# Kernel tuning notes

Measured on AMD Instinct MI355X. Metric: run time of the kernel, lower is better.

Reference implementation:

```python
import jax, jax.numpy as jnp
import numpy as np
import math

B, S, D, H = 4, 1024, 1024, 16
DK = D // H
HID = 2 * D
EPS = 1e-5

def _lin(key, din, dout):
    kw, kb = jax.random.split(key)
    sc = 1.0 / math.sqrt(din)
    return (jax.random.uniform(kw, (din, dout), jnp.float32, -sc, sc),
            jax.random.uniform(kb, (dout,), jnp.float32, -sc, sc))

def setup_inputs() -> dict:
    key = jax.random.key(0)
    ks = jax.random.split(key, 10)
    x = jax.random.normal(ks[0], (B, S, D), jnp.float32)
    y = jax.random.normal(ks[1], (B, S, D), jnp.float32)
    # additive causal mask (zeros below/on diag, -1e9 above)
    mask = jnp.where(jnp.tril(jnp.ones((S, S), bool)), 0.0, -1e9).astype(jnp.float32)
    qkv_w, qkv_b = _lin(ks[2], D, 3 * D)
    ao_w, ao_b = _lin(ks[3], D, D)
    kv_w, kv_b = _lin(ks[4], D, 2 * D)
    q_w, q_b = _lin(ks[5], D, D)
    co_w, co_b = _lin(ks[6], D, D)
    fc1_w, fc1_b = _lin(ks[7], D, HID)
    fc2_w, fc2_b = _lin(ks[8], HID, D)
    g = jnp.ones((D,), jnp.float32)
    b = jnp.zeros((D,), jnp.float32)
    return dict(x=x, y=y, mask=mask,
                qkv_w=qkv_w, qkv_b=qkv_b, ao_w=ao_w, ao_b=ao_b,
                kv_w=kv_w, kv_b=kv_b, q_w=q_w, q_b=q_b, co_w=co_w, co_b=co_b,
                fc1_w=fc1_w, fc1_b=fc1_b, fc2_w=fc2_w, fc2_b=fc2_b,
                ln1_g=g, ln1_b=b, ln2_g=g, ln2_b=b, ln3_g=g, ln3_b=b)

def _heads(t):  # [B,S,D] -> [B,H,S,DK]
    return t.reshape(B, S, H, -1).transpose(0, 2, 1, 3)

def _merge(t):  # [B,H,S,DK] -> [B,S,D]
    return t.transpose(0, 2, 1, 3).reshape(B, S, D)

def _attn(q, k, v, mask):
    scores = jnp.einsum('bhqd,bhkd->bhqk', q, k) / math.sqrt(q.shape[-1])
    if mask is not None:
        scores = scores + mask
    p = jax.nn.softmax(scores, axis=-1)
    return jnp.einsum('bhqk,bhkd->bhqd', p, v)

def _ln(t, g, b):
    mu = jnp.mean(t, axis=-1, keepdims=True)
    var = jnp.mean(jnp.square(t - mu), axis=-1, keepdims=True)
    return (t - mu) / jnp.sqrt(var + EPS) * g + b

def reference(x, y, mask, qkv_w, qkv_b, ao_w, ao_b, kv_w, kv_b, q_w, q_b,
              co_w, co_b, fc1_w, fc1_b, fc2_w, fc2_b,
              ln1_g, ln1_b, ln2_g, ln2_b, ln3_g, ln3_b):
    # masked self-attention on y
    qkv = y @ qkv_w + qkv_b
    qh, kh, vh = jnp.split(_heads(qkv), 3, axis=-1)
    sa = _merge(_attn(qh, kh, vh, mask)) @ ao_w + ao_b
    y_att = _ln(sa + y, ln1_g, ln1_b)  # dropout is identity (eval)
    # cross-attention: kv from x, q from ORIGINAL y (as in source), no mask
    kv = _heads(x @ kv_w + kv_b)
    ck, cv = jnp.split(kv, 2, axis=-1)
    cq = _heads(y @ q_w + q_b)
    cross = _merge(_attn(cq, ck, cv, None)) @ co_w + co_b
    # quirk in source: LN applied BEFORE residual add here
    y_cross = _ln(cross, ln2_g, ln2_b) + y_att
    # feedforward (hidden = 2*d_model)
    ff = jax.nn.relu(y_cross @ fc1_w + fc1_b) @ fc2_w + fc2_b
    return _ln(ff + y_cross, ln3_g, ln3_b)
```

## Files before the change

### kernel.cpp

```cpp
#include <hip/hip_runtime.h>
#include <cstdint>
#include <cstddef>


#define DEV __device__ __forceinline__

typedef __bf16 bf16x8 __attribute__((ext_vector_type(8)));
typedef float f32x4 __attribute__((ext_vector_type(4)));

DEV float bf2f(uint16_t h) { return __builtin_bit_cast(float, (uint32_t)h << 16); }
DEV uint16_t f2bf(float f) {
  uint32_t u = __builtin_bit_cast(uint32_t, f);
  return (uint16_t)((u + 0x7fffu + ((u >> 16) & 1u)) >> 16);
}

DEV void gload16(const void* g, void* l) {
  __builtin_amdgcn_global_load_lds((const __attribute__((address_space(1))) void*)g,
                                   (__attribute__((address_space(3))) void*)l, 16, 0, 0);
}

__global__ __launch_bounds__(256) void cvt_f2b(const float* __restrict__ in,
                                               uint16_t* __restrict__ out, int n4) {
  const int i = blockIdx.x * 256 + threadIdx.x;
  if (i < n4) {
    const float4 v = ((const float4*)in)[i];
    const uint32_t w0 = (uint32_t)f2bf(v.x) | ((uint32_t)f2bf(v.y) << 16);
    const uint32_t w1 = (uint32_t)f2bf(v.z) | ((uint32_t)f2bf(v.w) << 16);
    ((uint2*)out)[i] = make_uint2(w0, w1);
  }
}

__global__ __launch_bounds__(256) void ktranspose(const float* __restrict__ W,
                                                  uint16_t* __restrict__ Wt,
                                                  int K, int N) {
  __shared__ float t[32][33];
  const int tx = threadIdx.x & 31, ty = threadIdx.x >> 5;
  const int n0 = blockIdx.x * 32, k0 = blockIdx.y * 32;
#pragma unroll
  for (int i = 0; i < 32; i += 8)
    t[ty + i][tx] = W[(size_t)(k0 + ty + i) * N + n0 + tx];
  __syncthreads();
#pragma unroll
  for (int i = 0; i < 32; i += 8)
    Wt[(size_t)(n0 + ty + i) * K + k0 + tx] = f2bf(t[tx][ty + i]);
}

enum { EP_QKV = 0, EP_RES_F32RES, EP_SCKV, EP_Q, EP_F32, EP_RELU, EP_RES_B16RES };

template <int EPI>
__global__ __launch_bounds__(256) void gemm_bt(const uint16_t* __restrict__ A,
                                               const uint16_t* __restrict__ Bt,
                                               const float* __restrict__ bias,
                                               void* __restrict__ out0,
                                               const void* __restrict__ res,
                                               int M, int N, int K) {
  __shared__ __align__(16) uint16_t As[128 * 32];
  __shared__ __align__(16) uint16_t Bs[128 * 32];
  const int tid = threadIdx.x;
  const int wid = tid >> 6, lane = tid & 63;
  const int g = lane >> 4, lr = lane & 15;
  const int wr = wid >> 1, wc = wid & 1;
  const int m0 = blockIdx.y * 128, n0 = blockIdx.x * 128;

  const char* Ab = (const char*)A;
  const char* Bb = (const char*)Bt;
  const size_t rs = (size_t)K * 2;

  const int rc = lane >> 2;
  const int scb = ((lane & 3) << 4) ^ ((rc & 3) << 4);

  int aoff[4], boff[4];
#pragma unroll
  for (int m = 0; m < 4; ++m) {
    const int row = wr * 64 + m * 16 + lr;
    aoff[m] = row * 64 + ((g * 16) ^ ((row & 3) << 4));
  }
#pragma unroll
  for (int n = 0; n < 4; ++n) {
    const int row = wc * 64 + n * 16 + lr;
    boff[n] = row * 64 + ((g * 16) ^ ((row & 3) << 4));
  }

  f32x4 acc[4][4] = {};
  const int nk = K >> 5;
  for (int kt = 0; kt < nk; ++kt) {
    __syncthreads();
#pragma unroll
    for (int i = 0; i < 2; ++i) {
      const int c = wid * 2 + i;
      gload16(Ab + (size_t)(m0 + c * 16 + rc) * rs + (size_t)kt * 64 + scb,
              (void*)((char*)As + c * 1024));
      gload16(Bb + (size_t)(n0 + c * 16 + rc) * rs + (size_t)kt * 64 + scb,
              (void*)((char*)Bs + c * 1024));
    }
    asm volatile("s_waitcnt vmcnt(0)" ::: "memory");
    __syncthreads();

    bf16x8 av[4], bv[4];
#pragma unroll
    for (int m = 0; m < 4; ++m) av[m] = *(const bf16x8*)((const char*)As + aoff[m]);
#pragma unroll
    for (int n = 0; n < 4; ++n) bv[n] = *(const bf16x8*)((const char*)Bs + boff[n]);
#pragma unroll
    for (int m = 0; m < 4; ++m)
#pragma unroll
      for (int n = 0; n < 4; ++n)
        acc[m][n] = __builtin_amdgcn_mfma_f32_16x16x32_bf16(av[m], bv[n], acc[m][n], 0, 0, 0);
  }

#pragma unroll
  for (int m = 0; m < 4; ++m) {
#pragma unroll
    for (int n = 0; n < 4; ++n) {
      const int gcol = n0 + wc * 64 + n * 16 + lr;
      const float bb = bias[gcol];
#pragma unroll
      for (int r = 0; r < 4; ++r) {
        const int grow = m0 + wr * 64 + m * 16 + g * 4 + r;
        float v = acc[m][n][r] + bb;
        if constexpr (EPI == EP_QKV) {
          const int b = grow >> 10, s = grow & 1023;
          const int h = gcol / 192;
          const int rr = gcol - h * 192;
          const int part = rr >> 6, d = rr & 63;
          const int bh = b * 16 + h;
          uint16_t* base = (uint16_t*)out0;
          if (part == 2)
            base[2u * 4194304u + ((size_t)bh * 64 + d) * 1024 + s] = f2bf(v);
          else
            base[(size_t)part * 4194304u + ((size_t)bh * 1024 + s) * 64 + d] = f2bf(v);
        } else if constexpr (EPI == EP_SCKV) {
          const int b = grow >> 10, s = grow & 1023;
          const int h = gcol >> 7, part = (gcol >> 6) & 1, d = gcol & 63;
          const int bh = b * 16 + h;
          uint16_t* base = (uint16_t*)out0;
          if (part == 0)
            base[((size_t)bh * 1024 + s) * 64 + d] = f2bf(v);
          else
            base[4194304u + ((size_t)bh * 64 + d) * 1024 + s] = f2bf(v);
        } else if constexpr (EPI == EP_Q) {
          const int b = grow >> 10, s = grow & 1023;
          const int h = gcol >> 6, d = gcol & 63;
          ((uint16_t*)out0)[((size_t)(b * 16 + h) * 1024 + s) * 64 + d] = f2bf(v);
        } else if constexpr (EPI == EP_RES_F32RES) {
          v += ((const float*)res)[(size_t)grow * N + gcol];
          ((float*)out0)[(size_t)grow * N + gcol] = v;
        } else if constexpr (EPI == EP_F32) {
          ((float*)out0)[(size_t)grow * N + gcol] = v;
        } else if constexpr (EPI == EP_RELU) {
          ((uint16_t*)out0)[(size_t)grow * N + gcol] = f2bf(v > 0.f ? v : 0.f);
        } else if constexpr (EPI == EP_RES_B16RES) {
          v += bf2f(((const uint16_t*)res)[(size_t)grow * N + gcol]);
          ((float*)out0)[(size_t)grow * N + gcol] = v;
        }
      }
    }
  }
}

template <bool CAUSAL>
__global__ __launch_bounds__(256) void attn_fused(const uint16_t* __restrict__ Qp,
                                                  const uint16_t* __restrict__ Kp,
                                                  const uint16_t* __restrict__ Vtp,
                                                  uint16_t* __restrict__ O) {
  __shared__ __align__(16) uint16_t Kl[64 * 64];
  __shared__ __align__(16) uint16_t Vl[64 * 64];
  __shared__ __align__(16) uint16_t Pl[4][16 * 64];
  const int tid = threadIdx.x, wid = tid >> 6, lane = tid & 63;
  const int g = lane >> 4, lr = lane & 15;
  const int qb = blockIdx.x, bh = blockIdx.y;
  const char* Qb = (const char*)(Qp + (size_t)bh * 65536);
  const char* Kb = (const char*)(Kp + (size_t)bh * 65536);
  const char* Vb = (const char*)(Vtp + (size_t)bh * 65536);
  const int q0 = qb * 64 + wid * 16;

  bf16x8 aq[2];
#pragma unroll
  for (int ks = 0; ks < 2; ++ks)
    aq[ks] = *(const bf16x8*)(Qb + ((size_t)(q0 + lr) * 64 + ks * 32 + g * 8) * 2);

  float m_run[4], l_run[4];
  f32x4 oacc[4] = {};
#pragma unroll
  for (int r = 0; r < 4; ++r) { m_run[r] = -1e30f; l_run[r] = 0.f; }

  const int rc = lane >> 3;
  const int scb = ((lane & 7) << 4) ^ (rc << 4);
  const int nkt = CAUSAL ? (qb + 1) : 16;

  for (int kt = 0; kt < nkt; ++kt) {
    __syncthreads();
#pragma unroll
    for (int i = 0; i < 2; ++i) {
      const int c = wid * 2 + i;
      gload16(Kb + (size_t)(kt * 64 + c * 8 + rc) * 128 + scb, (void*)((char*)Kl + c * 1024));
      gload16(Vb + (size_t)(c * 8 + rc) * 2048 + kt * 128 + scb, (void*)((char*)Vl + c * 1024));
    }
    asm volatile("s_waitcnt vmcnt(0)" ::: "memory");
    __syncthreads();

    f32x4 sc[4];
#pragma unroll
    for (int n = 0; n < 4; ++n) {
      f32x4 t = {};
#pragma unroll
      for (int ks = 0; ks < 2; ++ks) {
        const int row = n * 16 + lr;
        bf16x8 bk = *(const bf16x8*)((const char*)Kl + row * 128 +
                                     ((ks * 64 + g * 16) ^ ((row & 7) << 4)));
        t = __builtin_amdgcn_mfma_f32_16x16x32_bf16(aq[ks], bk, t, 0, 0, 0);
      }
      sc[n] = t;
    }
    float p[4][4];
#pragma unroll
    for (int n = 0; n < 4; ++n)
#pragma unroll
      for (int r = 0; r < 4; ++r) {
        float v = sc[n][r] * 0.125f;
        if (CAUSAL) {
          const int k_abs = kt * 64 + n * 16 + lr;
          const int q_abs = q0 + g * 4 + r;
          if (k_abs > q_abs) v = -1e9f;
        }
        p[n][r] = v;
      }
#pragma unroll
    for (int r = 0; r < 4; ++r) {
      float mx = fmaxf(fmaxf(p[0][r], p[1][r]), fmaxf(p[2][r], p[3][r]));
      mx = fmaxf(mx, __shfl_xor(mx, 1));
      mx = fmaxf(mx, __shfl_xor(mx, 2));
      mx = fmaxf(mx, __shfl_xor(mx, 4));
      mx = fmaxf(mx, __shfl_xor(mx, 8));
      const float mnew = fmaxf(m_run[r], mx);
      const float f = __expf(m_run[r] - mnew);
      m_run[r] = mnew;
      float ls = 0.f;
#pragma unroll
      for (int n = 0; n < 4; ++n) {
        const float e = __expf(p[n][r] - mnew);
        p[n][r] = e;
        ls += e;
      }
      ls += __shfl_xor(ls, 1);
      ls += __shfl_xor(ls, 2);
      ls += __shfl_xor(ls, 4);
      ls += __shfl_xor(ls, 8);
      l_run[r] = l_run[r] * f + ls;
#pragma unroll
      for (int n = 0; n < 4; ++n) oacc[n][r] *= f;
    }
    char* Pb = (char*)Pl[wid];
#pragma unroll
    for (int n = 0; n < 4; ++n)
#pragma unroll
      for (int r = 0; r < 4; ++r) {
        const int row = g * 4 + r;
        *(uint16_t*)(Pb + row * 128 + ((n * 32 + lr * 2) ^ ((row & 7) << 4))) = f2bf(p[n][r]);
      }
    asm volatile("s_waitcnt lgkmcnt(0)" ::: "memory");
#pragma unroll
    for (int ks = 0; ks < 2; ++ks) {
      bf16x8 pa = *(const bf16x8*)(Pb + lr * 128 + ((ks * 64 + g * 16) ^ ((lr & 7) << 4)));
#pragma unroll
      for (int n2 = 0; n2 < 4; ++n2) {
        const int row = n2 * 16 + lr;
        bf16x8 bv = *(const bf16x8*)((const char*)Vl + row * 128 +
                                     ((ks * 64 + g * 16) ^ ((row & 7) << 4)));
        oacc[n2] = __builtin_amdgcn_mfma_f32_16x16x32_bf16(pa, bv, oacc[n2], 0, 0, 0);
      }
    }
  }

  const int b = bh >> 4, h = bh & 15;
#pragma unroll
  for (int n2 = 0; n2 < 4; ++n2)
#pragma unroll
    for (int r = 0; r < 4; ++r) {
      const int q = q0 + g * 4 + r, d = n2 * 16 + lr;
      const float v = oacc[n2][r] / l_run[r];
      O[(size_t)(b * 1024 + q) * 1024 + h * 64 + d] = f2bf(v);
    }
}

__global__ __launch_bounds__(256) void ln_kernel(const float* __restrict__ in,
                                                 const float* __restrict__ gam,
                                                 const float* __restrict__ bet,
                                                 const float* __restrict__ addend,
                                                 float* __restrict__ outf,
                                                 uint16_t* __restrict__ outb) {
  __shared__ float red[4];
  const int tid = threadIdx.x;
  const size_t row = blockIdx.x;
  const float4 v = ((const float4*)(in + row * 1024))[tid];
  float s = v.x + v.y + v.z + v.w;
#pragma unroll
  for (int o = 1; o < 64; o <<= 1) s += __shfl_xor(s, o);
  const int wid = tid >> 6, lane = tid & 63;
  if (lane == 0) red[wid] = s;
  __syncthreads();
  s = red[0] + red[1] + red[2] + red[3];
  const float mu = s * (1.f / 1024.f);
  const float d0 = v.x - mu, d1 = v.y - mu, d2 = v.z - mu, d3 = v.w - mu;
  float sq = d0 * d0 + d1 * d1 + d2 * d2 + d3 * d3;
  __syncthreads();
#pragma unroll
  for (int o = 1; o < 64; o <<= 1) sq += __shfl_xor(sq, o);
  if (lane == 0) red[wid] = sq;
  __syncthreads();
  sq = red[0] + red[1] + red[2] + red[3];
  const float inv = rsqrtf(sq * (1.f / 1024.f) + 1e-5f);
  const float4 gv = ((const float4*)(gam))[tid];
  const float4 bv = ((const float4*)(bet))[tid];
  float o0 = d0 * inv * gv.x + bv.x;
  float o1 = d1 * inv * gv.y + bv.y;
  float o2 = d2 * inv * gv.z + bv.z;
  float o3 = d3 * inv * gv.w + bv.w;
  if (addend) {
    const float4 a = ((const float4*)(addend + row * 1024))[tid];
    o0 += a.x; o1 += a.y; o2 += a.z; o3 += a.w;
  }
  if (outf)
    ((float4*)(outf + row * 1024))[tid] = make_float4(o0, o1, o2, o3);
  if (outb) {
    const uint32_t w0 = (uint32_t)f2bf(o0) | ((uint32_t)f2bf(o1) << 16);
    const uint32_t w1 = (uint32_t)f2bf(o2) | ((uint32_t)f2bf(o3) << 16);
    ((uint2*)(outb + row * 1024))[tid] = make_uint2(w0, w1);
  }
}

extern "C" void kernel_launch(void* const* d_in, const int* in_sizes, int n_in,
                              void* d_out, int out_size, void* d_ws, size_t ws_size,
                              hipStream_t stream) {
  (void)in_sizes; (void)n_in; (void)out_size; (void)ws_size;
  const float* x     = (const float*)d_in[0];
  const float* y     = (const float*)d_in[1];
  const float* qkv_w = (const float*)d_in[3];
  const float* qkv_b = (const float*)d_in[4];
  const float* ao_w  = (const float*)d_in[5];
  const float* ao_b  = (const float*)d_in[6];
  const float* kv_w  = (const float*)d_in[7];
  const float* kv_b  = (const float*)d_in[8];
  const float* q_w   = (const float*)d_in[9];
  const float* q_b   = (const float*)d_in[10];
  const float* co_w  = (const float*)d_in[11];
  const float* co_b  = (const float*)d_in[12];
  const float* fc1_w = (const float*)d_in[13];
  const float* fc1_b = (const float*)d_in[14];
  const float* fc2_w = (const float*)d_in[15];
  const float* fc2_b = (const float*)d_in[16];
  const float* ln1_g = (const float*)d_in[17];
  const float* ln1_b = (const float*)d_in[18];
  const float* ln2_g = (const float*)d_in[19];
  const float* ln2_b = (const float*)d_in[20];
  const float* ln3_g = (const float*)d_in[21];
  const float* ln3_b = (const float*)d_in[22];

  char* ws = (char*)d_ws;
  size_t off = 0;
  auto alloc = [&](size_t bytes) {
    char* p = ws + off;
    off += (bytes + 255) & ~(size_t)255;
    return p;
  };
  uint16_t* xb     = (uint16_t*)alloc(4194304ull * 2);
  uint16_t* yb     = (uint16_t*)alloc(4194304ull * 2);
  uint16_t* wT_qkv = (uint16_t*)alloc(3072ull * 1024 * 2);
  uint16_t* wT_ao  = (uint16_t*)alloc(1024ull * 1024 * 2);
  uint16_t* wT_kv  = (uint16_t*)alloc(2048ull * 1024 * 2);
  uint16_t* wT_q   = (uint16_t*)alloc(1024ull * 1024 * 2);
  uint16_t* wT_co  = (uint16_t*)alloc(1024ull * 1024 * 2);
  uint16_t* wT_fc1 = (uint16_t*)alloc(2048ull * 1024 * 2);
  uint16_t* wT_fc2 = (uint16_t*)alloc(1024ull * 2048 * 2);
  uint16_t* QKV    = (uint16_t*)alloc(3ull * 4194304 * 2);
  uint16_t* SA     = (uint16_t*)alloc(4194304ull * 2);
  float*    YATT   = (float*)alloc(4194304ull * 4);
  float*    TMP    = (float*)alloc(4194304ull * 4);
  uint16_t* YCB    = (uint16_t*)alloc(4194304ull * 2);

  const dim3 blk(256);

  cvt_f2b<<<dim3(4096), blk, 0, stream>>>(x, xb, 1048576);
  cvt_f2b<<<dim3(4096), blk, 0, stream>>>(y, yb, 1048576);

  ktranspose<<<dim3(96, 32), blk, 0, stream>>>(qkv_w, wT_qkv, 1024, 3072);
  ktranspose<<<dim3(32, 32), blk, 0, stream>>>(ao_w, wT_ao, 1024, 1024);
  ktranspose<<<dim3(64, 32), blk, 0, stream>>>(kv_w, wT_kv, 1024, 2048);
  ktranspose<<<dim3(32, 32), blk, 0, stream>>>(q_w, wT_q, 1024, 1024);
  ktranspose<<<dim3(32, 32), blk, 0, stream>>>(co_w, wT_co, 1024, 1024);
  ktranspose<<<dim3(64, 32), blk, 0, stream>>>(fc1_w, wT_fc1, 1024, 2048);
  ktranspose<<<dim3(32, 64), blk, 0, stream>>>(fc2_w, wT_fc2, 2048, 1024);

  gemm_bt<EP_QKV><<<dim3(24, 32), blk, 0, stream>>>(yb, wT_qkv, qkv_b, QKV, nullptr, 4096, 3072, 1024);
  attn_fused<true><<<dim3(16, 64), blk, 0, stream>>>(QKV, QKV + 4194304, QKV + 2 * 4194304, SA);
  gemm_bt<EP_RES_F32RES><<<dim3(8, 32), blk, 0, stream>>>(SA, wT_ao, ao_b, TMP, y, 4096, 1024, 1024);
  ln_kernel<<<dim3(4096), blk, 0, stream>>>(TMP, ln1_g, ln1_b, nullptr, YATT, nullptr);
  gemm_bt<EP_SCKV><<<dim3(16, 32), blk, 0, stream>>>(xb, wT_kv, kv_b, QKV + 4194304, nullptr, 4096, 2048, 1024);
  gemm_bt<EP_Q><<<dim3(8, 32), blk, 0, stream>>>(yb, wT_q, q_b, QKV, nullptr, 4096, 1024, 1024);
  attn_fused<false><<<dim3(16, 64), blk, 0, stream>>>(QKV, QKV + 4194304, QKV + 2 * 4194304, SA);
  gemm_bt<EP_F32><<<dim3(8, 32), blk, 0, stream>>>(SA, wT_co, co_b, TMP, nullptr, 4096, 1024, 1024);
  ln_kernel<<<dim3(4096), blk, 0, stream>>>(TMP, ln2_g, ln2_b, YATT, nullptr, YCB);
  gemm_bt<EP_RELU><<<dim3(16, 32), blk, 0, stream>>>(YCB, wT_fc1, fc1_b, (uint16_t*)YATT, nullptr, 4096, 2048, 1024);
  gemm_bt<EP_RES_B16RES><<<dim3(8, 32), blk, 0, stream>>>((const uint16_t*)YATT, wT_fc2, fc2_b, TMP, YCB, 4096, 1024, 2048);
  ln_kernel<<<dim3(4096), blk, 0, stream>>>(TMP, ln3_g, ln3_b, nullptr, (float*)d_out, nullptr);
}
```

Measured before the change: 560.0 us.

## Merge prep launches and stream K/V directly from global in attention

Merges the two input-conversion kernels and seven weight-transpose kernels into a single prep launch that dispatches on block index, which removes launch overhead. In attention, K and V tiles are no longer staged through LDS with block-wide barriers. Each wave reads its MFMA operands straight from global memory (relying on L1/L2 reuse across the four waves), and on the causal diagonal tile it skips the score MFMAs for fully masked 16-column blocks. The risk is redundant global traffic, since all four waves load the same K/V, and higher load latency without LDS staging.

```diff
diff --git a/kernel.cpp b/kernel.cpp
--- a/kernel.cpp
+++ b/kernel.cpp
@@ -19,30 +19,48 @@
                                    (__attribute__((address_space(3))) void*)l, 16, 0, 0);
 }
 
-__global__ __launch_bounds__(256) void cvt_f2b(const float* __restrict__ in,
-                                               uint16_t* __restrict__ out, int n4) {
-  const int i = blockIdx.x * 256 + threadIdx.x;
-  if (i < n4) {
-    const float4 v = ((const float4*)in)[i];
-    const uint32_t w0 = (uint32_t)f2bf(v.x) | ((uint32_t)f2bf(v.y) << 16);
-    const uint32_t w1 = (uint32_t)f2bf(v.z) | ((uint32_t)f2bf(v.w) << 16);
-    ((uint2*)out)[i] = make_uint2(w0, w1);
-  }
-}
-
-__global__ __launch_bounds__(256) void ktranspose(const float* __restrict__ W,
-                                                  uint16_t* __restrict__ Wt,
-                                                  int K, int N) {
+__global__ __launch_bounds__(256) void prep(
+    const float* __restrict__ x, const float* __restrict__ y,
+    uint16_t* __restrict__ xb, uint16_t* __restrict__ yb,
+    const float* __restrict__ w0, uint16_t* __restrict__ t0,
+    const float* __restrict__ w1, uint16_t* __restrict__ t1,
+    const float* __restrict__ w2, uint16_t* __restrict__ t2,
+    const float* __restrict__ w3, uint16_t* __restrict__ t3,
+    const float* __restrict__ w4, uint16_t* __restrict__ t4,
+    const float* __restrict__ w5, uint16_t* __restrict__ t5,
+    const float* __restrict__ w6, uint16_t* __restrict__ t6) {
+  int bid = blockIdx.x;
+  const int tid = threadIdx.x;
+  if (bid < 8192) {
+    const float* src = (bid < 4096) ? x : y;
+    uint16_t* dst = (bid < 4096) ? xb : yb;
+    const int i = (bid & 4095) * 256 + tid;
+    const float4 v = ((const float4*)src)[i];
+    const uint32_t lo = (uint32_t)f2bf(v.x) | ((uint32_t)f2bf(v.y) << 16);
+    const uint32_t hi = (uint32_t)f2bf(v.z) | ((uint32_t)f2bf(v.w) << 16);
+    ((uint2*)dst)[i] = make_uint2(lo, hi);
+    return;
+  }
+  bid -= 8192;
+  const float* W; uint16_t* T; int K, N, tile;
+  if (bid < 3072)       { W = w0; T = t0; K = 1024; N = 3072; tile = bid; }
+  else if (bid < 4096)  { W = w1; T = t1; K = 1024; N = 1024; tile = bid - 3072; }
+  else if (bid < 6144)  { W = w2; T = t2; K = 1024; N = 2048; tile = bid - 4096; }
+  else if (bid < 7168)  { W = w3; T = t3; K = 1024; N = 1024; tile = bid - 6144; }
+  else if (bid < 8192)  { W = w4; T = t4; K = 1024; N = 1024; tile = bid - 7168; }
+  else if (bid < 10240) { W = w5; T = t5; K = 1024; N = 2048; tile = bid - 8192; }
+  else                  { W = w6; T = t6; K = 2048; N = 1024; tile = bid - 10240; }
+  const int ntx = N >> 5;
+  const int n0 = (tile % ntx) * 32, k0 = (tile / ntx) * 32;
   __shared__ float t[32][33];
-  const int tx = threadIdx.x & 31, ty = threadIdx.x >> 5;
-  const int n0 = blockIdx.x * 32, k0 = blockIdx.y * 32;
+  const int tx = tid & 31, ty = tid >> 5;
 #pragma unroll
   for (int i = 0; i < 32; i += 8)
     t[ty + i][tx] = W[(size_t)(k0 + ty + i) * N + n0 + tx];
   __syncthreads();
 #pragma unroll
   for (int i = 0; i < 32; i += 8)
-    Wt[(size_t)(n0 + ty + i) * K + k0 + tx] = f2bf(t[tx][ty + i]);
+    T[(size_t)(n0 + ty + i) * K + k0 + tx] = f2bf(t[tx][ty + i]);
 }
 
 enum { EP_QKV = 0, EP_RES_F32RES, EP_SCKV, EP_Q, EP_F32, EP_RELU, EP_RES_B16RES };
@@ -163,8 +181,6 @@
                                                   const uint16_t* __restrict__ Kp,
                                                   const uint16_t* __restrict__ Vtp,
                                                   uint16_t* __restrict__ O) {
-  __shared__ __align__(16) uint16_t Kl[64 * 64];
-  __shared__ __align__(16) uint16_t Vl[64 * 64];
   __shared__ __align__(16) uint16_t Pl[4][16 * 64];
   const int tid = threadIdx.x, wid = tid >> 6, lane = tid & 63;
   const int g = lane >> 4, lr = lane & 15;
@@ -184,34 +200,34 @@
 #pragma unroll
   for (int r = 0; r < 4; ++r) { m_run[r] = -1e30f; l_run[r] = 0.f; }
 
-  const int rc = lane >> 3;
-  const int scb = ((lane & 7) << 4) ^ (rc << 4);
   const int nkt = CAUSAL ? (qb + 1) : 16;
+  char* Pb = (char*)Pl[wid];
 
   for (int kt = 0; kt < nkt; ++kt) {
-    __syncthreads();
-#pragma unroll
-    for (int i = 0; i < 2; ++i) {
-      const int c = wid * 2 + i;
-      gload16(Kb + (size_t)(kt * 64 + c * 8 + rc) * 128 + scb, (void*)((char*)Kl + c * 1024));
-      gload16(Vb + (size_t)(c * 8 + rc) * 2048 + kt * 128 + scb, (void*)((char*)Vl + c * 1024));
-    }
-    asm volatile("s_waitcnt vmcnt(0)" ::: "memory");
-    __syncthreads();
+    const int nlim = (CAUSAL && kt == qb) ? wid : 3;
+
+    bf16x8 bk[4][2];
+#pragma unroll
+    for (int n = 0; n < 4; ++n)
+      if (n <= nlim)
+#pragma unroll
+        for (int ks = 0; ks < 2; ++ks)
+          bk[n][ks] = *(const bf16x8*)(Kb + ((size_t)(kt * 64 + n * 16 + lr) * 64 + ks * 32 + g * 8) * 2);
 
     f32x4 sc[4];
 #pragma unroll
     for (int n = 0; n < 4; ++n) {
-      f32x4 t = {};
-#pragma unroll
-      for (int ks = 0; ks < 2; ++ks) {
-        const int row = n * 16 + lr;
-        bf16x8 bk = *(const bf16x8*)((const char*)Kl + row * 128 +
-                                     ((ks * 64 + g * 16) ^ ((row & 7) << 4)));
-        t = __builtin_amdgcn_mfma_f32_16x16x32_bf16(aq[ks], bk, t, 0, 0, 0);
-      }
-      sc[n] = t;
-    }
+      if (n <= nlim) {
+        f32x4 t = {};
+#pragma unroll
+        for (int ks = 0; ks < 2; ++ks)
+          t = __builtin_amdgcn_mfma_f32_16x16x32_bf16(aq[ks], bk[n][ks], t, 0, 0, 0);
+        sc[n] = t;
+      } else {
+        sc[n] = f32x4{-1e10f, -1e10f, -1e10f, -1e10f};
+      }
+    }
+
     float p[4][4];
 #pragma unroll
     for (int n = 0; n < 4; ++n)
@@ -250,7 +266,6 @@
 #pragma unroll
       for (int n = 0; n < 4; ++n) oacc[n][r] *= f;
     }
-    char* Pb = (char*)Pl[wid];
 #pragma unroll
     for (int n = 0; n < 4; ++n)
 #pragma unroll
@@ -264,9 +279,7 @@
       bf16x8 pa = *(const bf16x8*)(Pb + lr * 128 + ((ks * 64 + g * 16) ^ ((lr & 7) << 4)));
 #pragma unroll
       for (int n2 = 0; n2 < 4; ++n2) {
-        const int row = n2 * 16 + lr;
-        bf16x8 bv = *(const bf16x8*)((const char*)Vl + row * 128 +
-                                     ((ks * 64 + g * 16) ^ ((row & 7) << 4)));
+        bf16x8 bv = *(const bf16x8*)(Vb + ((size_t)(n2 * 16 + lr) * 1024 + kt * 64 + ks * 32 + g * 8) * 2);
         oacc[n2] = __builtin_amdgcn_mfma_f32_16x16x32_bf16(pa, bv, oacc[n2], 0, 0, 0);
       }
     }
@@ -380,16 +393,9 @@
 
   const dim3 blk(256);
 
-  cvt_f2b<<<dim3(4096), blk, 0, stream>>>(x, xb, 1048576);
-  cvt_f2b<<<dim3(4096), blk, 0, stream>>>(y, yb, 1048576);
-
-  ktranspose<<<dim3(96, 32), blk, 0, stream>>>(qkv_w, wT_qkv, 1024, 3072);
-  ktranspose<<<dim3(32, 32), blk, 0, stream>>>(ao_w, wT_ao, 1024, 1024);
-  ktranspose<<<dim3(64, 32), blk, 0, stream>>>(kv_w, wT_kv, 1024, 2048);
-  ktranspose<<<dim3(32, 32), blk, 0, stream>>>(q_w, wT_q, 1024, 1024);
-  ktranspose<<<dim3(32, 32), blk, 0, stream>>>(co_w, wT_co, 1024, 1024);
-  ktranspose<<<dim3(64, 32), blk, 0, stream>>>(fc1_w, wT_fc1, 1024, 2048);
-  ktranspose<<<dim3(32, 64), blk, 0, stream>>>(fc2_w, wT_fc2, 2048, 1024);
+  prep<<<dim3(20480), blk, 0, stream>>>(x, y, xb, yb,
+                                        qkv_w, wT_qkv, ao_w, wT_ao, kv_w, wT_kv,
+                                        q_w, wT_q, co_w, wT_co, fc1_w, wT_fc1, fc2_w, wT_fc2);
 
   gemm_bt<EP_QKV><<<dim3(24, 32), blk, 0, stream>>>(yb, wT_qkv, qkv_b, QKV, nullptr, 4096, 3072, 1024);
   attn_fused<true><<<dim3(16, 64), blk, 0, stream>>>(QKV, QKV + 4194304, QKV + 2 * 4194304, SA);
```

Measured after the change: 668.7 us. 19.4% more time.
